# Kernel optimization log

Hardware: AMD Instinct MI355X
Metric: run time of the kernel (lower is better)

Reference implementation:

```python
import jax, jax.numpy as jnp
import numpy as np

B, N, D, S, ITERS = 64, 2048, 256, 8, 3
SCALE = D ** -0.5
EPS_LN = 1e-5

def _ln(x, g, b):
    m = jnp.mean(x, axis=-1, keepdims=True)
    v = jnp.var(x, axis=-1, keepdims=True)
    return (x - m) / jnp.sqrt(v + EPS_LN) * g + b

def setup_inputs() -> dict:
    key = jax.random.key(0)
    ks = jax.random.split(key, 20)
    s = D ** -0.5
    f32 = jnp.float32
    return dict(
        x=jax.random.normal(ks[0], (B, N, D), f32),
        noise=jax.random.normal(ks[1], (B, S, D), f32),
        slots_mu=jax.random.normal(ks[2], (1, 1, D), f32),
        slots_sigma=jax.random.normal(ks[3], (1, 1, D), f32),
        Wq=jax.random.normal(ks[4], (D, D), f32) * s, bq=jnp.zeros((D,), f32),
        Wk=jax.random.normal(ks[5], (D, D), f32) * s, bk=jnp.zeros((D,), f32),
        Wv=jax.random.normal(ks[6], (D, D), f32) * s, bv=jnp.zeros((D,), f32),
        W_ih=jax.random.normal(ks[7], (3 * D, D), f32) * s, b_ih=jnp.zeros((3 * D,), f32),
        W_hh=jax.random.normal(ks[8], (3 * D, D), f32) * s, b_hh=jnp.zeros((3 * D,), f32),
        W1=jax.random.normal(ks[9], (D, D), f32) * s, b1=jnp.zeros((D,), f32),
        W2=jax.random.normal(ks[10], (D, D), f32) * s, b2=jnp.zeros((D,), f32),
        g_in=jnp.ones((D,), f32), be_in=jnp.zeros((D,), f32),
        g_sl=jnp.ones((D,), f32), be_sl=jnp.zeros((D,), f32),
        g_ff=jnp.ones((D,), f32), be_ff=jnp.zeros((D,), f32),
    )

def reference(x, noise, slots_mu, slots_sigma, Wq, bq, Wk, bk, Wv, bv,
              W_ih, b_ih, W_hh, b_hh, W1, b1, W2, b2,
              g_in, be_in, g_sl, be_sl, g_ff, be_ff):
    # slot init: mu + softplus(sigma) * noise  -> [B,S,D]
    slots = slots_mu + jax.nn.softplus(slots_sigma) * noise
    xn = _ln(x, g_in, be_in)
    k = xn @ Wk.T + bk  # [B,N,D]
    v = xn @ Wv.T + bv
    for _ in range(ITERS):
        prev = slots
        q = _ln(slots, g_sl, be_sl) @ Wq.T + bq  # [B,S,D]
        logits = jnp.einsum('bsd,bnd->bsn', q, k) * SCALE
        attn = jax.nn.softmax(logits, axis=-1) + 1e-8  # softmax over inputs, as in source
        attn = attn / jnp.sum(attn, axis=-1, keepdims=True)
        updates = jnp.einsum('bsn,bnd->bsd', attn, v)
        # GRUCell(input=updates, hidden=prev); torch gate order r,z,n
        gi = updates @ W_ih.T + b_ih
        gh = prev @ W_hh.T + b_hh
        ir, iz, i_n = jnp.split(gi, 3, axis=-1)
        hr, hz, h_n = jnp.split(gh, 3, axis=-1)
        r = jax.nn.sigmoid(ir + hr)
        z = jax.nn.sigmoid(iz + hz)
        n = jnp.tanh(i_n + r * h_n)
        slots = (1.0 - z) * n + z * prev
        # residual MLP
        h = jax.nn.relu(_ln(slots, g_ff, be_ff) @ W1.T + b1)
        slots = slots + (h @ W2.T + b2)
    return slots
```

## Files before the change

kernel.cpp:

```cpp
#include <hip/hip_runtime.h>
#include <cstddef>


#define BB 64
#define NN 2048
#define DD 256
#define NCH 8
#define CHK 256
#define NITER 3
#define XPITCH 264

typedef unsigned short u16;
typedef unsigned int u32;
typedef _Float16 h2 __attribute__((ext_vector_type(2)));
typedef _Float16 h4 __attribute__((ext_vector_type(4)));

#if defined(__has_builtin)
#if __has_builtin(__builtin_amdgcn_fdot2)
#define HAS_FDOT2 1
#endif
#endif

#ifdef HAS_FDOT2
#define FDOT2(a,b,c) __builtin_amdgcn_fdot2((a),(b),(c),false)
#else
#define FDOT2(a,b,c) fmaf((float)(a).y,(float)(b).y, fmaf((float)(a).x,(float)(b).x,(c)))
#endif

__device__ __forceinline__ h2 u2h2(u32 v){ union{u32 u; h2 h;} c; c.u=v; return c.h; }

__global__ __launch_bounds__(256) void kA(const float* __restrict__ x, const float* __restrict__ g_in,
                                          const float* __restrict__ be_in, u16* __restrict__ xn,
                                          const float* __restrict__ noise, const float* __restrict__ mu,
                                          const float* __restrict__ sig, float* __restrict__ S,
                                          const float* __restrict__ Wq, const float* __restrict__ Wk,
                                          const float* __restrict__ bq, const float* __restrict__ Wih,
                                          const float* __restrict__ Wv, const float* __restrict__ bv,
                                          const float* __restrict__ bih,
                                          float* __restrict__ Wqk, float* __restrict__ bqk,
                                          float* __restrict__ Wihv, float* __restrict__ bihv){
  __shared__ float col[256];
  const int t = threadIdx.x;
  const int blk = blockIdx.x;
  if(blk < 256){
    col[t] = Wq[t*256 + blk];
    __syncthreads();
    float acc = 0.f;
    #pragma unroll 4
    for(int j=0;j<256;j++) acc += col[j]*Wk[j*256+t];
    Wqk[blk*256+t] = acc * 0.0625f;
  } else if(blk < 1024){
    int c = blk - 256;
    col[t] = Wih[c*256+t];
    __syncthreads();
    float acc = 0.f;
    #pragma unroll 4
    for(int j=0;j<256;j++) acc += col[j]*Wv[j*256+t];
    Wihv[(size_t)c*256+t] = acc;
  } else if(blk < 1536){
    int i = (blk-1024)*256 + t;
    float sg = sig[t];
    float sp = fmaxf(sg, 0.f) + log1pf(expf(-fabsf(sg)));
    S[i] = mu[t] + sp * noise[i];
  } else if(blk == 1536){
    float acc = 0.f;
    for(int j=0;j<256;j++) acc += bq[j]*Wk[j*256+t];
    bqk[t] = acc * 0.0625f;
  } else if(blk == 1537){
    for(int c=t;c<768;c+=256){
      float acc = 0.f;
      for(int j=0;j<256;j++) acc += Wih[c*256+j]*bv[j];
      bihv[c] = acc + bih[c];
    }
  } else {
    int wave = t>>6, lane = t&63;
    size_t row = (size_t)(blk-1538)*4 + wave;
    float4 v = *(const float4*)(x + row*256 + lane*4);
    float s1 = v.x+v.y+v.z+v.w;
    float s2 = v.x*v.x + v.y*v.y + v.z*v.z + v.w*v.w;
    #pragma unroll
    for(int off=1; off<64; off<<=1){ s1 += __shfl_xor(s1,off); s2 += __shfl_xor(s2,off); }
    float m = s1*(1.f/256.f);
    float var = s2*(1.f/256.f) - m*m;
    float rs = rsqrtf(var + 1e-5f);
    float4 gg = *(const float4*)(g_in + lane*4);
    float4 bb = *(const float4*)(be_in + lane*4);
    union { h4 h; ushort4 s4; } pk;
    pk.h[0] = (_Float16)((v.x-m)*rs*gg.x + bb.x);
    pk.h[1] = (_Float16)((v.y-m)*rs*gg.y + bb.y);
    pk.h[2] = (_Float16)((v.z-m)*rs*gg.z + bb.z);
    pk.h[3] = (_Float16)((v.w-m)*rs*gg.w + bb.w);
    *(ushort4*)(xn + row*256 + lane*4) = pk.s4;
  }
}

__global__ __launch_bounds__(256) void kB(const float* __restrict__ Wihv, const float* __restrict__ Whh,
                                          const float* __restrict__ W1, const float* __restrict__ W2,
                                          float* __restrict__ WihvT, float* __restrict__ WhhT,
                                          float* __restrict__ W1T, float* __restrict__ W2T,
                                          const float* __restrict__ S0, const float* __restrict__ g_sl,
                                          const float* __restrict__ be_sl, const float* __restrict__ Wqk,
                                          const float* __restrict__ bqk, float* __restrict__ Qq){
  __shared__ float tile[64][65];
  __shared__ float lnA[8][256];
  const int blk = blockIdx.x, t = threadIdx.x;
  if(blk < 128){
    const float* src; float* dst; int R, C, tb;
    if(blk < 48){ src=Wihv; dst=WihvT; R=768; C=256; tb=blk; }
    else if(blk < 96){ src=Whh; dst=WhhT; R=768; C=256; tb=blk-48; }
    else if(blk < 112){ src=W1; dst=W1T; R=256; C=256; tb=blk-96; }
    else { src=W2; dst=W2T; R=256; C=256; tb=blk-112; }
    const int tilesC = C/64;
    const int r0 = (tb/tilesC)*64, c0 = (tb%tilesC)*64;
    const int x = t&63, y = t>>6;
    #pragma unroll
    for(int k=0;k<16;k++) tile[y*16+k][x] = src[(size_t)(r0+y*16+k)*C + c0+x];
    __syncthreads();
    #pragma unroll
    for(int k=0;k<16;k++) dst[(size_t)(c0+y*16+k)*R + r0+x] = tile[x][y*16+k];
    return;
  }
  const int w = t>>6, l = t&63;
  const int r0 = (blk-128)*8;
  #pragma unroll
  for(int rr=0; rr<2; rr++){
    int r = w*2 + rr;
    float4 v = *(const float4*)(S0 + (size_t)(r0+r)*256 + l*4);
    float s1 = v.x+v.y+v.z+v.w;
    float s2 = v.x*v.x+v.y*v.y+v.z*v.z+v.w*v.w;
    #pragma unroll
    for(int off=1; off<64; off<<=1){ s1 += __shfl_xor(s1,off); s2 += __shfl_xor(s2,off); }
    float m = s1*(1.f/256.f);
    float var = s2*(1.f/256.f) - m*m;
    float rs = rsqrtf(var + 1e-5f);
    float4 gg = *(const float4*)(g_sl + l*4);
    float4 bb = *(const float4*)(be_sl + l*4);
    float4 o;
    o.x=(v.x-m)*rs*gg.x+bb.x; o.y=(v.y-m)*rs*gg.y+bb.y;
    o.z=(v.z-m)*rs*gg.z+bb.z; o.w=(v.w-m)*rs*gg.w+bb.w;
    *(float4*)(&lnA[r][l*4]) = o;
  }
  __syncthreads();
  const int c4 = l*4;
  float acc[2][4] = {};
  #pragma unroll 2
  for(int k=0;k<256;k++){
    float4 wv = *(const float4*)(Wqk + (size_t)k*256 + c4);
    float a0 = lnA[2*w][k], a1 = lnA[2*w+1][k];
    acc[0][0]+=a0*wv.x; acc[0][1]+=a0*wv.y; acc[0][2]+=a0*wv.z; acc[0][3]+=a0*wv.w;
    acc[1][0]+=a1*wv.x; acc[1][1]+=a1*wv.y; acc[1][2]+=a1*wv.z; acc[1][3]+=a1*wv.w;
  }
  float4 bq4 = *(const float4*)(bqk + c4);
  #pragma unroll
  for(int rr=0; rr<2; rr++){
    float4 o;
    o.x=acc[rr][0]+bq4.x; o.y=acc[rr][1]+bq4.y; o.z=acc[rr][2]+bq4.z; o.w=acc[rr][3]+bq4.w;
    *(float4*)(Qq + (size_t)(r0+2*w+rr)*256 + c4) = o;
  }
}

__global__ __launch_bounds__(512) void k_attn(const float* __restrict__ Qq, const u16* __restrict__ xn,
                                              float* __restrict__ mP, float* __restrict__ lP,
                                              float* __restrict__ aP){
  __shared__ __align__(16) u16 xs[256*XPITCH];
  __shared__ h2 qs[8][128];
  __shared__ float plT[8][256];
  __shared__ float mS[8], lS[8];
  const int b = blockIdx.x, c = blockIdx.y, t = threadIdx.x;
  const int w = t>>6, l = t&63;
  {
    const uint4* xg4 = (const uint4*)(xn + ((size_t)b*NN + (size_t)c*CHK)*DD);
    #pragma unroll
    for(int k=0;k<16;k++){
      int idx = t + 512*k;
      int n = idx>>5, j = idx&31;
      *(uint4*)(xs + (size_t)n*XPITCH + j*8) = xg4[idx];
    }
  }
  for(int i=t; i<1024; i+=512){
    int s = i>>7, p = i&127;
    float a = Qq[b*2048 + s*256 + 2*p];
    float bq = Qq[b*2048 + s*256 + 2*p + 1];
    h2 hv; hv.x = (_Float16)a; hv.y = (_Float16)bq;
    qs[s][p] = hv;
  }
  __syncthreads();
  const int n = t & 255, sg = t >> 8;
  float lg[4]={0,0,0,0};
  {
    const u16* xr = xs + (size_t)n*XPITCH;
    #pragma unroll 4
    for(int d8=0; d8<32; ++d8){
      uint4 u = *(const uint4*)(xr + d8*8);
      h2 xa=u2h2(u.x), xb=u2h2(u.y), xc=u2h2(u.z), xd=u2h2(u.w);
      #pragma unroll
      for(int k=0;k<4;k++){
        const h2* qp = &qs[sg*4+k][d8*4];
        float acc = lg[k];
        acc = FDOT2(xa, qp[0], acc);
        acc = FDOT2(xb, qp[1], acc);
        acc = FDOT2(xc, qp[2], acc);
        acc = FDOT2(xd, qp[3], acc);
        lg[k] = acc;
      }
    }
    #pragma unroll
    for(int k=0;k<4;k++) plT[sg*4+k][n] = lg[k];
  }
  __syncthreads();
  {
    float mx = -1e30f;
    #pragma unroll
    for(int k=0;k<4;k++) mx = fmaxf(mx, plT[w][l + 64*k]);
    #pragma unroll
    for(int off=1; off<64; off<<=1) mx = fmaxf(mx, __shfl_xor(mx, off));
    if(l==0) mS[w] = mx;
  }
  __syncthreads();
  #pragma unroll
  for(int k=0;k<4;k++) plT[sg*4+k][n] = __expf(lg[k] - mS[sg*4+k]);
  __syncthreads();
  {
    float sm = 0.f;
    #pragma unroll
    for(int k=0;k<4;k++) sm += plT[w][l + 64*k];
    #pragma unroll
    for(int off=1; off<64; off<<=1) sm += __shfl_xor(sm, off);
    if(l==0) lS[w] = sm;
  }
  __syncthreads();
  const size_t pb = (size_t)(b*NCH + c)*8;
  {
    float4 a4 = {0.f,0.f,0.f,0.f};
    const u16* xq = xs + 4*l;
    #pragma unroll 8
    for(int nn=0; nn<256; ++nn){
      uint2 u = *(const uint2*)(xq + (size_t)nn*XPITCH);
      h2 ha=u2h2(u.x), hb=u2h2(u.y);
      float p = plT[w][nn];
      a4.x += p*(float)ha.x; a4.y += p*(float)ha.y;
      a4.z += p*(float)hb.x; a4.w += p*(float)hb.y;
    }
    *(float4*)(aP + (pb + w)*256 + l*4) = a4;
  }
  if(t<8){ mP[pb+t] = mS[t]; lP[pb+t] = lS[t]; }
}

__global__ __launch_bounds__(512) void k_post(const float* __restrict__ mP, const float* __restrict__ lP,
                                              const float* __restrict__ aP, const float* __restrict__ WihvT,
                                              const float* __restrict__ bihv, const float* __restrict__ WhhT,
                                              const float* __restrict__ bhh, const float* __restrict__ Sc,
                                              const float* __restrict__ g_ff, const float* __restrict__ be_ff,
                                              const float* __restrict__ W1T, const float* __restrict__ b1,
                                              const float* __restrict__ W2T, const float* __restrict__ b2,
                                              const float* __restrict__ g_sl, const float* __restrict__ be_sl,
                                              const float* __restrict__ Wqk, const float* __restrict__ bqk,
                                              float* __restrict__ Sout, float* __restrict__ Qq, int writeQ){
  __shared__ float Ut[256], Sp[256], Gt[2][768];
  __shared__ float Row[256], Ht[256], Snew[256], Lq[256], Hp[2][256];
  __shared__ float red2[2][4];
  const int t = threadIdx.x;
  const int c = t&255, h = t>>8, w4 = (t>>6)&3, l = t&63;
  const int r = blockIdx.x;
  const int b = r>>3, s = r&7;
  if(t < 256){
    const float* mpb = mP + b*64 + s;
    const float* lpb = lP + b*64 + s;
    float M = -1e30f;
    #pragma unroll
    for(int c8=0;c8<8;c8++) M = fmaxf(M, mpb[c8*8]);
    float wc[8]; float L = 0.f;
    #pragma unroll
    for(int c8=0;c8<8;c8++){ wc[c8] = __expf(mpb[c8*8] - M); L += lpb[c8*8]*wc[c8]; }
    float inv = 1.f/L;
    size_t base = ((size_t)b*64 + s)*256 + c;
    float u = 0.f;
    #pragma unroll
    for(int c8=0;c8<8;c8++) u += wc[c8]*aP[base + (size_t)c8*2048];
    Ut[c] = u*inv;
    Sp[c] = Sc[(size_t)r*256 + c];
  }
  __syncthreads();
  if(t < 384){
    const int mat = t/192, q4 = (t - mat*192)*4;
    const float* WT = mat ? WhhT : WihvT;
    const float* bb = mat ? bhh : bihv;
    const float* A  = mat ? Sp : Ut;
    float4 acc = *(const float4*)(bb + q4);
    const float* wp = WT + q4;
    #pragma unroll 8
    for(int d=0; d<256; ++d){
      float4 wv = *(const float4*)(wp + (size_t)d*768);
      float a = A[d];
      acc.x += a*wv.x; acc.y += a*wv.y; acc.z += a*wv.z; acc.w += a*wv.w;
    }
    *(float4*)(&Gt[mat][q4]) = acc;
  }
  __syncthreads();
  if(t < 256){
    float gir = Gt[0][c], giz = Gt[0][256+c], gin = Gt[0][512+c];
    float ghr = Gt[1][c], ghz = Gt[1][256+c], ghn = Gt[1][512+c];
    float rr = 1.f/(1.f + __expf(-(gir+ghr)));
    float zz = 1.f/(1.f + __expf(-(giz+ghz)));
    float nn = tanhf(gin + rr*ghn);
    float sp = (1.f-zz)*nn + zz*Sp[c];
    Ut[c] = sp;
    float s1 = sp, s2 = sp*sp;
    #pragma unroll
    for(int off=1; off<64; off<<=1){ s1 += __shfl_xor(s1,off); s2 += __shfl_xor(s2,off); }
    if(l==0){ red2[0][w4] = s1; red2[1][w4] = s2; }
  }
  __syncthreads();
  if(t < 256){
    float t1 = red2[0][0]+red2[0][1]+red2[0][2]+red2[0][3];
    float t2 = red2[1][0]+red2[1][1]+red2[1][2]+red2[1][3];
    float m = t1*(1.f/256.f);
    float var = t2*(1.f/256.f) - m*m;
    float rs = rsqrtf(var + 1e-5f);
    Row[c] = (Ut[c]-m)*rs*g_ff[c] + be_ff[c];
  }
  __syncthreads();
  {
    const float* w1 = W1T + (size_t)h*128*256 + c;
    float acc = h ? 0.f : b1[c];
    const float* rw = &Row[h*128];
    #pragma unroll 8
    for(int d=0; d<128; ++d) acc += rw[d]*w1[(size_t)d*256];
    Hp[h][c] = acc;
  }
  __syncthreads();
  if(t < 256) Ht[c] = fmaxf(Hp[0][c]+Hp[1][c], 0.f);
  __syncthreads();
  {
    const float* w2 = W2T + (size_t)h*128*256 + c;
    float acc = h ? 0.f : b2[c];
    const float* hw = &Ht[h*128];
    #pragma unroll 8
    for(int d=0; d<128; ++d) acc += hw[d]*w2[(size_t)d*256];
    Hp[h][c] = acc;
  }
  __syncthreads();
  if(t < 256){
    float sn = Hp[0][c]+Hp[1][c] + Ut[c];
    Sout[(size_t)r*256 + c] = sn;
    Snew[c] = sn;
  }
  if(writeQ){
    __syncthreads();
    if(t < 256){
      float sn = Snew[c];
      float s1 = sn, s2 = sn*sn;
      #pragma unroll
      for(int off=1; off<64; off<<=1){ s1 += __shfl_xor(s1,off); s2 += __shfl_xor(s2,off); }
      if(l==0){ red2[0][w4] = s1; red2[1][w4] = s2; }
    }
    __syncthreads();
    if(t < 256){
      float t1 = red2[0][0]+red2[0][1]+red2[0][2]+red2[0][3];
      float t2 = red2[1][0]+red2[1][1]+red2[1][2]+red2[1][3];
      float m = t1*(1.f/256.f);
      float var = t2*(1.f/256.f) - m*m;
      float rs = rsqrtf(var + 1e-5f);
      Lq[c] = (Snew[c]-m)*rs*g_sl[c] + be_sl[c];
    }
    __syncthreads();
    {
      const float* wq = Wqk + (size_t)h*128*256 + c;
      float acc = h ? 0.f : bqk[c];
      const float* lw = &Lq[h*128];
      #pragma unroll 8
      for(int d=0; d<128; ++d) acc += lw[d]*wq[(size_t)d*256];
      Hp[h][c] = acc;
    }
    __syncthreads();
    if(t < 256) Qq[(size_t)r*256 + c] = Hp[0][c]+Hp[1][c];
  }
}

extern "C" void kernel_launch(void* const* d_in, const int* in_sizes, int n_in,
                              void* d_out, int out_size, void* d_ws, size_t ws_size,
                              hipStream_t stream){
  const float* x    = (const float*)d_in[0];
  const float* noise= (const float*)d_in[1];
  const float* mu   = (const float*)d_in[2];
  const float* sig  = (const float*)d_in[3];
  const float* Wq   = (const float*)d_in[4];
  const float* bq   = (const float*)d_in[5];
  const float* Wk   = (const float*)d_in[6];
  const float* Wv   = (const float*)d_in[8];
  const float* bv   = (const float*)d_in[9];
  const float* W_ih = (const float*)d_in[10];
  const float* b_ih = (const float*)d_in[11];
  const float* W_hh = (const float*)d_in[12];
  const float* b_hh = (const float*)d_in[13];
  const float* W1m  = (const float*)d_in[14];
  const float* b1v  = (const float*)d_in[15];
  const float* W2m  = (const float*)d_in[16];
  const float* b2v  = (const float*)d_in[17];
  const float* g_in = (const float*)d_in[18];
  const float* be_in= (const float*)d_in[19];
  const float* g_sl = (const float*)d_in[20];
  const float* be_sl= (const float*)d_in[21];
  const float* g_ff = (const float*)d_in[22];
  const float* be_ff= (const float*)d_in[23];

  char* p = (char*)d_ws;
  auto alloc = [&](size_t bytes)->char*{ char* q = p; p += (bytes + 255) & ~(size_t)255; return q; };
  u16*   xn    = (u16*)  alloc((size_t)BB*NN*DD*2);
  float* Wqk   = (float*)alloc(256*256*4);
  float* bqk   = (float*)alloc(256*4);
  float* Wihv  = (float*)alloc((size_t)768*256*4);
  float* WihvT = (float*)alloc((size_t)256*768*4);
  float* bihv  = (float*)alloc(768*4);
  float* WhhT  = (float*)alloc((size_t)256*768*4);
  float* W1T   = (float*)alloc(256*256*4);
  float* W2T   = (float*)alloc(256*256*4);
  float* S0    = (float*)alloc(512*256*4);
  float* S1    = (float*)alloc(512*256*4);
  float* Qq    = (float*)alloc(512*256*4);
  float* mP    = (float*)alloc(64*NCH*8*4);
  float* lP    = (float*)alloc(64*NCH*8*4);
  float* aP    = (float*)alloc((size_t)64*NCH*8*256*4);
  if((size_t)(p - (char*)d_ws) > ws_size) return;

  kA<<<34306, 256, 0, stream>>>(x, g_in, be_in, xn, noise, mu, sig, S0,
                                Wq, Wk, bq, W_ih, Wv, bv, b_ih, Wqk, bqk, Wihv, bihv);
  kB<<<192, 256, 0, stream>>>(Wihv, W_hh, W1m, W2m, WihvT, WhhT, W1T, W2T,
                              S0, g_sl, be_sl, Wqk, bqk, Qq);

  float* Sin = S0;
  float* Sping[2] = { S1, S0 };
  for(int it=0; it<NITER; ++it){
    float* Sout = (it==NITER-1) ? (float*)d_out : Sping[it&1];
    k_attn<<<dim3(64, NCH), 512, 0, stream>>>(Qq, xn, mP, lP, aP);
    k_post<<<512, 512, 0, stream>>>(mP, lP, aP, WihvT, bihv, WhhT, b_hh, Sin, g_ff, be_ff,
                                    W1T, b1v, W2T, b2v, g_sl, be_sl, Wqk, bqk,
                                    Sout, Qq, (it<NITER-1) ? 1 : 0);
    Sin = Sout;
  }
}
```

Measured before the change: 328.0 us.

## Process four slot rows per k_post block to reuse weight loads

k_post now handles four slot rows per block instead of one, so each weight element read from global memory (GRU, MLP and query matrices) is applied to four activation rows. The grid shrinks from 512 to 128 blocks, and a shared-memory union overlays the gate buffers with the LayerNorm and MLP buffers. This cuts repeated weight traffic per row, at the cost of fewer blocks to hide latency and more registers per thread.

```diff
diff --git a/kernel.cpp b/kernel.cpp
--- a/kernel.cpp
+++ b/kernel.cpp
@@ -246,6 +246,11 @@
   if(t<8){ mP[pb+t] = mS[t]; lP[pb+t] = lS[t]; }
 }
 
+union PostU {
+  float Gt[2][4][768];
+  struct { float Row[4][256]; float Ht[4][256]; float Lq[4][256]; } m;
+};
+
 __global__ __launch_bounds__(512) void k_post(const float* __restrict__ mP, const float* __restrict__ lP,
                                               const float* __restrict__ aP, const float* __restrict__ WihvT,
                                               const float* __restrict__ bihv, const float* __restrict__ WhhT,
@@ -256,16 +261,24 @@
                                               const float* __restrict__ g_sl, const float* __restrict__ be_sl,
                                               const float* __restrict__ Wqk, const float* __restrict__ bqk,
                                               float* __restrict__ Sout, float* __restrict__ Qq, int writeQ){
-  __shared__ float Ut[256], Sp[256], Gt[2][768];
-  __shared__ float Row[256], Ht[256], Snew[256], Lq[256], Hp[2][256];
-  __shared__ float red2[2][4];
+  __shared__ float Ut[4][256];
+  __shared__ float Sp[4][256];
+  __shared__ float Hp[2][4][256];
+  __shared__ PostU uu;
+  __shared__ float red2[4][2];
   const int t = threadIdx.x;
-  const int c = t&255, h = t>>8, w4 = (t>>6)&3, l = t&63;
-  const int r = blockIdx.x;
-  const int b = r>>3, s = r&7;
-  if(t < 256){
-    const float* mpb = mP + b*64 + s;
-    const float* lpb = lP + b*64 + s;
+  const int r0 = blockIdx.x*4;
+  const int b = r0>>3;
+  const int w = t>>6, l = t&63;
+  const int c = t&255, hh = t>>8;
+
+  #pragma unroll
+  for(int k=0;k<2;k++){
+    int idx = t + 512*k;
+    int r = idx>>8, cc = idx&255;
+    int rr = r0 + r, ss = rr&7;
+    const float* mpb = mP + b*64 + ss;
+    const float* lpb = lP + b*64 + ss;
     float M = -1e30f;
     #pragma unroll
     for(int c8=0;c8<8;c8++) M = fmaxf(M, mpb[c8*8]);
@@ -273,107 +286,162 @@
     #pragma unroll
     for(int c8=0;c8<8;c8++){ wc[c8] = __expf(mpb[c8*8] - M); L += lpb[c8*8]*wc[c8]; }
     float inv = 1.f/L;
-    size_t base = ((size_t)b*64 + s)*256 + c;
+    size_t base = ((size_t)b*64 + ss)*256 + cc;
     float u = 0.f;
     #pragma unroll
     for(int c8=0;c8<8;c8++) u += wc[c8]*aP[base + (size_t)c8*2048];
-    Ut[c] = u*inv;
-    Sp[c] = Sc[(size_t)r*256 + c];
-  }
-  __syncthreads();
+    Ut[r][cc] = u*inv;
+    Sp[r][cc] = Sc[(size_t)rr*256 + cc];
+  }
+  __syncthreads();
+
   if(t < 384){
     const int mat = t/192, q4 = (t - mat*192)*4;
     const float* WT = mat ? WhhT : WihvT;
-    const float* bb = mat ? bhh : bihv;
-    const float* A  = mat ? Sp : Ut;
-    float4 acc = *(const float4*)(bb + q4);
+    const float* bb2 = mat ? bhh : bihv;
+    const float (*A)[256] = mat ? Sp : Ut;
+    float4 bias4 = *(const float4*)(bb2 + q4);
+    float4 ac0 = bias4, ac1 = bias4, ac2 = bias4, ac3 = bias4;
     const float* wp = WT + q4;
-    #pragma unroll 8
+    #pragma unroll 4
     for(int d=0; d<256; ++d){
       float4 wv = *(const float4*)(wp + (size_t)d*768);
-      float a = A[d];
-      acc.x += a*wv.x; acc.y += a*wv.y; acc.z += a*wv.z; acc.w += a*wv.w;
-    }
-    *(float4*)(&Gt[mat][q4]) = acc;
+      float a0=A[0][d], a1=A[1][d], a2=A[2][d], a3=A[3][d];
+      ac0.x += a0*wv.x; ac0.y += a0*wv.y; ac0.z += a0*wv.z; ac0.w += a0*wv.w;
+      ac1.x += a1*wv.x; ac1.y += a1*wv.y; ac1.z += a1*wv.z; ac1.w += a1*wv.w;
+      ac2.x += a2*wv.x; ac2.y += a2*wv.y; ac2.z += a2*wv.z; ac2.w += a2*wv.w;
+      ac3.x += a3*wv.x; ac3.y += a3*wv.y; ac3.z += a3*wv.z; ac3.w += a3*wv.w;
+    }
+    *(float4*)(&uu.Gt[mat][0][q4]) = ac0;
+    *(float4*)(&uu.Gt[mat][1][q4]) = ac1;
+    *(float4*)(&uu.Gt[mat][2][q4]) = ac2;
+    *(float4*)(&uu.Gt[mat][3][q4]) = ac3;
+  }
+  __syncthreads();
+
+  #pragma unroll
+  for(int k=0;k<2;k++){
+    int idx = t + 512*k;
+    int r = idx>>8, cc = idx&255;
+    float gir = uu.Gt[0][r][cc], giz = uu.Gt[0][r][256+cc], gin = uu.Gt[0][r][512+cc];
+    float ghr = uu.Gt[1][r][cc], ghz = uu.Gt[1][r][256+cc], ghn = uu.Gt[1][r][512+cc];
+    float rr2 = 1.f/(1.f + __expf(-(gir+ghr)));
+    float zz = 1.f/(1.f + __expf(-(giz+ghz)));
+    float nn = tanhf(gin + rr2*ghn);
+    Ut[r][cc] = (1.f-zz)*nn + zz*Sp[r][cc];
+  }
+  __syncthreads();
+
+  if(w < 4){
+    float s1=0.f, s2=0.f;
+    #pragma unroll
+    for(int k2=0;k2<4;k2++){ float v = Ut[w][l + 64*k2]; s1 += v; s2 += v*v; }
+    #pragma unroll
+    for(int off=1; off<64; off<<=1){ s1 += __shfl_xor(s1,off); s2 += __shfl_xor(s2,off); }
+    if(l==0){
+      float m = s1*(1.f/256.f);
+      float var = s2*(1.f/256.f) - m*m;
+      red2[w][0] = m; red2[w][1] = rsqrtf(var + 1e-5f);
+    }
+  }
+  __syncthreads();
+  #pragma unroll
+  for(int k=0;k<2;k++){
+    int idx = t + 512*k;
+    int r = idx>>8, cc = idx&255;
+    uu.m.Row[r][cc] = (Ut[r][cc]-red2[r][0])*red2[r][1]*g_ff[cc] + be_ff[cc];
+  }
+  __syncthreads();
+
+  {
+    const float* w1 = W1T + (size_t)hh*128*256 + c;
+    float a0 = hh ? 0.f : b1[c], a1=a0, a2=a0, a3=a0;
+    const int dB = hh*128;
+    #pragma unroll 8
+    for(int d=0; d<128; ++d){
+      float wv = w1[(size_t)d*256];
+      a0 += uu.m.Row[0][dB+d]*wv;
+      a1 += uu.m.Row[1][dB+d]*wv;
+      a2 += uu.m.Row[2][dB+d]*wv;
+      a3 += uu.m.Row[3][dB+d]*wv;
+    }
+    Hp[hh][0][c]=a0; Hp[hh][1][c]=a1; Hp[hh][2][c]=a2; Hp[hh][3][c]=a3;
+  }
+  __syncthreads();
+  #pragma unroll
+  for(int k=0;k<2;k++){
+    int idx = t + 512*k;
+    int r = idx>>8, cc = idx&255;
+    uu.m.Ht[r][cc] = fmaxf(Hp[0][r][cc]+Hp[1][r][cc], 0.f);
+  }
+  __syncthreads();
+
+  {
+    const float* w2 = W2T + (size_t)hh*128*256 + c;
+    float a0 = hh ? 0.f : b2[c], a1=a0, a2=a0, a3=a0;
+    const int dB = hh*128;
+    #pragma unroll 8
+    for(int d=0; d<128; ++d){
+      float wv = w2[(size_t)d*256];
+      a0 += uu.m.Ht[0][dB+d]*wv;
+      a1 += uu.m.Ht[1][dB+d]*wv;
+      a2 += uu.m.Ht[2][dB+d]*wv;
+      a3 += uu.m.Ht[3][dB+d]*wv;
+    }
+    Hp[hh][0][c]=a0; Hp[hh][1][c]=a1; Hp[hh][2][c]=a2; Hp[hh][3][c]=a3;
   }
   __syncthreads();
   if(t < 256){
-    float gir = Gt[0][c], giz = Gt[0][256+c], gin = Gt[0][512+c];
-    float ghr = Gt[1][c], ghz = Gt[1][256+c], ghn = Gt[1][512+c];
-    float rr = 1.f/(1.f + __expf(-(gir+ghr)));
-    float zz = 1.f/(1.f + __expf(-(giz+ghz)));
-    float nn = tanhf(gin + rr*ghn);
-    float sp = (1.f-zz)*nn + zz*Sp[c];
-    Ut[c] = sp;
-    float s1 = sp, s2 = sp*sp;
-    #pragma unroll
-    for(int off=1; off<64; off<<=1){ s1 += __shfl_xor(s1,off); s2 += __shfl_xor(s2,off); }
-    if(l==0){ red2[0][w4] = s1; red2[1][w4] = s2; }
-  }
-  __syncthreads();
-  if(t < 256){
-    float t1 = red2[0][0]+red2[0][1]+red2[0][2]+red2[0][3];
-    float t2 = red2[1][0]+red2[1][1]+red2[1][2]+red2[1][3];
-    float m = t1*(1.f/256.f);
-    float var = t2*(1.f/256.f) - m*m;
-    float rs = rsqrtf(var + 1e-5f);
-    Row[c] = (Ut[c]-m)*rs*g_ff[c] + be_ff[c];
-  }
-  __syncthreads();
-  {
-    const float* w1 = W1T + (size_t)h*128*256 + c;
-    float acc = h ? 0.f : b1[c];
-    const float* rw = &Row[h*128];
-    #pragma unroll 8
-    for(int d=0; d<128; ++d) acc += rw[d]*w1[(size_t)d*256];
-    Hp[h][c] = acc;
-  }
-  __syncthreads();
-  if(t < 256) Ht[c] = fmaxf(Hp[0][c]+Hp[1][c], 0.f);
-  __syncthreads();
-  {
-    const float* w2 = W2T + (size_t)h*128*256 + c;
-    float acc = h ? 0.f : b2[c];
-    const float* hw = &Ht[h*128];
-    #pragma unroll 8
-    for(int d=0; d<128; ++d) acc += hw[d]*w2[(size_t)d*256];
-    Hp[h][c] = acc;
-  }
-  __syncthreads();
-  if(t < 256){
-    float sn = Hp[0][c]+Hp[1][c] + Ut[c];
-    Sout[(size_t)r*256 + c] = sn;
-    Snew[c] = sn;
-  }
+    #pragma unroll
+    for(int r=0;r<4;r++){
+      float sn = Hp[0][r][c] + Hp[1][r][c] + Ut[r][c];
+      Sout[(size_t)(r0+r)*256 + c] = sn;
+      Ut[r][c] = sn;
+    }
+  }
+
   if(writeQ){
     __syncthreads();
-    if(t < 256){
-      float sn = Snew[c];
-      float s1 = sn, s2 = sn*sn;
+    if(w < 4){
+      float s1=0.f, s2=0.f;
+      #pragma unroll
+      for(int k2=0;k2<4;k2++){ float v = Ut[w][l + 64*k2]; s1 += v; s2 += v*v; }
       #pragma unroll
       for(int off=1; off<64; off<<=1){ s1 += __shfl_xor(s1,off); s2 += __shfl_xor(s2,off); }
-      if(l==0){ red2[0][w4] = s1; red2[1][w4] = s2; }
+      if(l==0){
+        float m = s1*(1.f/256.f);
+        float var = s2*(1.f/256.f) - m*m;
+        red2[w][0] = m; red2[w][1] = rsqrtf(var + 1e-5f);
+      }
+    }
+    __syncthreads();
+    #pragma unroll
+    for(int k=0;k<2;k++){
+      int idx = t + 512*k;
+      int r = idx>>8, cc = idx&255;
+      uu.m.Lq[r][cc] = (Ut[r][cc]-red2[r][0])*red2[r][1]*g_sl[cc] + be_sl[cc];
+    }
+    __syncthreads();
+    {
+      const float* wq = Wqk + (size_t)hh*128*256 + c;
+      float a0 = hh ? 0.f : bqk[c], a1=a0, a2=a0, a3=a0;
+      const int dB = hh*128;
+      #pragma unroll 8
+      for(int d=0; d<128; ++d){
+        float wv = wq[(size_t)d*256];
+        a0 += uu.m.Lq[0][dB+d]*wv;
+        a1 += uu.m.Lq[1][dB+d]*wv;
+        a2 += uu.m.Lq[2][dB+d]*wv;
+        a3 += uu.m.Lq[3][dB+d]*wv;
+      }
+      Hp[hh][0][c]=a0; Hp[hh][1][c]=a1; Hp[hh][2][c]=a2; Hp[hh][3][c]=a3;
     }
     __syncthreads();
     if(t < 256){
-      float t1 = red2[0][0]+red2[0][1]+red2[0][2]+red2[0][3];
-      float t2 = red2[1][0]+red2[1][1]+red2[1][2]+red2[1][3];
-      float m = t1*(1.f/256.f);
-      float var = t2*(1.f/256.f) - m*m;
-      float rs = rsqrtf(var + 1e-5f);
-      Lq[c] = (Snew[c]-m)*rs*g_sl[c] + be_sl[c];
-    }
-    __syncthreads();
-    {
-      const float* wq = Wqk + (size_t)h*128*256 + c;
-      float acc = h ? 0.f : bqk[c];
-      const float* lw = &Lq[h*128];
-      #pragma unroll 8
-      for(int d=0; d<128; ++d) acc += lw[d]*wq[(size_t)d*256];
-      Hp[h][c] = acc;
-    }
-    __syncthreads();
-    if(t < 256) Qq[(size_t)r*256 + c] = Hp[0][c]+Hp[1][c];
+      #pragma unroll
+      for(int r=0;r<4;r++)
+        Qq[(size_t)(r0+r)*256 + c] = Hp[0][r][c] + Hp[1][r][c];
+    }
   }
 }
 
@@ -433,7 +501,7 @@
   for(int it=0; it<NITER; ++it){
     float* Sout = (it==NITER-1) ? (float*)d_out : Sping[it&1];
     k_attn<<<dim3(64, NCH), 512, 0, stream>>>(Qq, xn, mP, lP, aP);
-    k_post<<<512, 512, 0, stream>>>(mP, lP, aP, WihvT, bihv, WhhT, b_hh, Sin, g_ff, be_ff,
+    k_post<<<128, 512, 0, stream>>>(mP, lP, aP, WihvT, bihv, WhhT, b_hh, Sin, g_ff, be_ff,
                                     W1T, b1v, W2T, b2v, g_sl, be_sl, Wqk, bqk,
                                     Sout, Qq, (it<NITER-1) ? 1 : 0);
     Sin = Sout;
```

Result: no change. 326.8 us (-0.4%).
